# Kernel optimization log

Measured on AMD Instinct MI355X. Metric: run time of the kernel, lower is better.

## Reference

```python
import jax, jax.numpy as jnp
import numpy as np
import math

B, S, D, NH, HFF, E, K, C, L, V = 8, 256, 1024, 16, 2048, 8, 2, 10, 4, 32000
HD = D // NH
EPS = 1e-5


def _pos_encoding(max_len, d_model):
    pos = jnp.arange(max_len, dtype=jnp.float32)[:, None]
    div = jnp.exp(jnp.arange(0, d_model, 2, dtype=jnp.float32) * (-math.log(10000.0) / d_model))
    pe = jnp.zeros((max_len, d_model), dtype=jnp.float32)
    pe = pe.at[:, 0::2].set(jnp.sin(pos * div))
    pe = pe.at[:, 1::2].set(jnp.cos(pos * div))
    return pe[:, None, :]  # [max_len, 1, D], matching torch buffer layout


def _layernorm(x, g, b):
    mu = jnp.mean(x, axis=-1, keepdims=True)
    var = jnp.mean((x - mu) ** 2, axis=-1, keepdims=True)
    return (x - mu) * jax.lax.rsqrt(var + EPS) * g + b


def setup_inputs() -> dict:
    key = jax.random.key(0)
    ks = jax.random.split(key, 20)
    sc = lambda *shape: 0.02
    inp = {
        "src": jax.random.randint(ks[0], (B, S), 0, V, dtype=jnp.int32),
        "emb": jax.random.normal(ks[1], (V, D), jnp.float32) * 0.02,
        "in_proj_w": jax.random.normal(ks[2], (L, 3 * D, D), jnp.float32) * 0.02,
        "in_proj_b": jnp.zeros((L, 3 * D), jnp.float32),
        "out_w": jax.random.normal(ks[3], (L, D, D), jnp.float32) * 0.02,
        "out_b": jnp.zeros((L, D), jnp.float32),
        "ln1_g": jnp.ones((L, D), jnp.float32),
        "ln1_b": jnp.zeros((L, D), jnp.float32),
        "ln2_g": jnp.ones((L, D), jnp.float32),
        "ln2_b": jnp.zeros((L, D), jnp.float32),
        "gate_w": jax.random.normal(ks[4], (L, E, D), jnp.float32) * 0.02,
        "gate_b": jnp.zeros((L, E), jnp.float32),
        "w1": jax.random.normal(ks[5], (L, E, D, HFF), jnp.float32) * 0.02,
        "b1": jnp.zeros((L, E, HFF), jnp.float32),
        "w2": jax.random.normal(ks[6], (L, E, HFF, D), jnp.float32) * 0.02,
        "b2": jnp.zeros((L, E, D), jnp.float32),
        "cls_w": jax.random.normal(ks[7], (C, D), jnp.float32) * 0.02,
        "cls_b": jnp.zeros((C,), jnp.float32),
    }
    return inp


def _attention(x, ipw, ipb, ow, ob):
    # x: [B,S,D]
    qkv = x @ ipw.T + ipb  # [B,S,3D]
    q, k, v = jnp.split(qkv, 3, axis=-1)
    q = q.reshape(B, S, NH, HD)
    k = k.reshape(B, S, NH, HD)
    v = v.reshape(B, S, NH, HD)
    scores = jnp.einsum("bqhd,bkhd->bhqk", q, k) / math.sqrt(HD)
    attn = jax.nn.softmax(scores, axis=-1)
    o = jnp.einsum("bhqk,bkhd->bqhd", attn, v).reshape(B, S, D)
    return o @ ow.T + ob


def _moe(x, gw, gb, w1, b1, w2, b2):
    # x: [B,S,D]; gw: [E,D]; w1: [E,D,H]; w2: [E,H,D]
    t = x.reshape(B * S, D)
    logits = t @ gw.T + gb  # [T,E]
    topv, topi = jax.lax.top_k(logits, K)  # [T,K]
    weights = jax.nn.softmax(topv, axis=-1)  # [T,K]
    # dense expert compute (small E, compute-bound), combine via top-k gather
    h = jax.nn.relu(jnp.einsum("td,edh->teh", t, w1) + b1)  # [T,E,H]
    y = jnp.einsum("teh,ehd->ted", h, w2) + b2  # [T,E,D]
    sel = jnp.take_along_axis(y, topi[:, :, None], axis=1)  # [T,K,D]
    out = jnp.sum(sel * weights[:, :, None], axis=1)  # [T,D]
    return out.reshape(B, S, D), logits.reshape(B, S, E)


def reference(src, emb, in_proj_w, in_proj_b, out_w, out_b, ln1_g, ln1_b,
              ln2_g, ln2_b, gate_w, gate_b, w1, b1, w2, b2, cls_w, cls_b):
    x = emb[src] * math.sqrt(D)  # [B,S,D]
    pe = _pos_encoding(5000, D)  # [max_len,1,D]
    # faithful to original: pe indexed by batch dim (x.size(0)), broadcast over seq
    x = x + pe[:B]  # [B,1,D] -> broadcast [B,S,D]
    all_gates = []
    for l in range(in_proj_w.shape[0]):
        a = _attention(x, in_proj_w[l], in_proj_b[l], out_w[l], out_b[l])
        x = _layernorm(x + a, ln1_g[l], ln1_b[l])
        m, g = _moe(x, gate_w[l], gate_b[l], w1[l], b1[l], w2[l], b2[l])
        x = _layernorm(x + m, ln2_g[l], ln2_b[l])
        all_gates.append(g)
    pooled = jnp.mean(x, axis=1)  # [B,D]
    out = pooled @ cls_w.T + cls_b  # [B,C]
    return out, jnp.stack(all_gates)  # ([B,C], [L,B,S,E])
```

## Files before the change

### kernel.cpp

```cpp
#include <hip/hip_runtime.h>
#include <math.h>

#define TKN 2048
#define DIM 1024
#define NHEAD 16
#define HDIM 64
#define HFF 2048
#define NE 8
#define TOPK 2
#define NCLS 10
#define NLAYER 4
#define SEQ 256
#define BATCH 8

typedef __attribute__((ext_vector_type(8))) _Float16 f16x8;
typedef __attribute__((ext_vector_type(4))) float f32x4;
typedef __attribute__((ext_vector_type(8))) unsigned short u16x8;

__device__ __forceinline__ unsigned short f2h(float v) {
  _Float16 h = (_Float16)v;
  return __builtin_bit_cast(unsigned short, h);
}
__device__ __forceinline__ float h2f(unsigned short u) {
  return (float)__builtin_bit_cast(_Float16, u);
}
__device__ __forceinline__ void fsplit(float v, unsigned short& hi, unsigned short& lo) {
  _Float16 h = (_Float16)v;
  hi = __builtin_bit_cast(unsigned short, h);
  lo = f2h(v - (float)h);
}

__device__ __forceinline__ void gload_lds16(const void* g, void* l) {
  __builtin_amdgcn_global_load_lds((__attribute__((address_space(1))) void*)g,
                                   (__attribute__((address_space(3))) void*)l,
                                   16, 0, 0);
}

__global__ __launch_bounds__(256) void k_embed(const int* __restrict__ src,
                                               const float* __restrict__ emb,
                                               float* __restrict__ x,
                                               unsigned short* __restrict__ xhi,
                                               unsigned short* __restrict__ xlo) {
  const int t = blockIdx.x;
  const int tid = threadIdx.x;
  const int b = t / SEQ;
  const int tok = src[t];
  const float* erow = emb + (size_t)tok * DIM;
  const size_t base = (size_t)t * DIM;
  const float cexp = -9.210340371976184f / 1024.0f;
#pragma unroll
  for (int j = 0; j < 4; ++j) {
    int d = tid + 256 * j;
    int i2 = d & ~1;
    float ang = (float)b * expf((float)i2 * cexp);
    float pe = (d & 1) ? cosf(ang) : sinf(ang);
    float v = erow[d] * 32.0f + pe;
    x[base + d] = v;
    fsplit(v, xhi[base + d], xlo[base + d]);
  }
}

template <bool LO>
__global__ __launch_bounds__(256) void k_cvt_split(const float* __restrict__ in,
                                                   unsigned short* __restrict__ ohi,
                                                   unsigned short* __restrict__ olo) {
  int i = blockIdx.x * 256 + threadIdx.x;
  float4 v = ((const float4*)in)[i];
  ushort4 h, l;
  fsplit(v.x, h.x, l.x); fsplit(v.y, h.y, l.y);
  fsplit(v.z, h.z, l.z); fsplit(v.w, h.w, l.w);
  ((ushort4*)ohi)[i] = h;
  if (LO) ((ushort4*)olo)[i] = l;
}

template <bool LO>
__global__ __launch_bounds__(256) void k_cvt_t2(const float* __restrict__ in,
                                                unsigned short* __restrict__ ohi,
                                                unsigned short* __restrict__ olo,
                                                int R, int Cc) {
  __shared__ float ts[64][33];
  const int t = threadIdx.x;
  const int c0 = blockIdx.x * 32, r0 = blockIdx.y * 64;
  const float* ip = in + (size_t)blockIdx.z * R * Cc;
  const size_t obase = (size_t)blockIdx.z * R * Cc;
  const int cc = t & 31, rr0 = t >> 5;
#pragma unroll
  for (int j = 0; j < 8; ++j)
    ts[rr0 + 8 * j][cc] = ip[(size_t)(r0 + rr0 + 8 * j) * Cc + c0 + cc];
  __syncthreads();
  const int c = t >> 3, rch = (t & 7) * 8;
  u16x8 hv, lv;
#pragma unroll
  for (int i = 0; i < 8; ++i) {
    unsigned short hi, lo;
    fsplit(ts[rch + i][c], hi, lo);
    hv[i] = hi; lv[i] = lo;
  }
  size_t o = obase + (size_t)(c0 + c) * R + r0 + rch;
  *(u16x8*)(ohi + o) = hv;
  if (LO) *(u16x8*)(olo + o) = lv;
}

template <int MODE, bool RELU, int OUTK, bool SPLIT>
__global__ __launch_bounds__(256) void k_mfma_gemm(
    const unsigned short* __restrict__ Ahi, const unsigned short* __restrict__ Alo,
    const unsigned short* __restrict__ Bhi, const unsigned short* __restrict__ Blo,
    const float* __restrict__ bias, void* __restrict__ out0, void* __restrict__ out1,
    int M, int N, int K,
    const int* __restrict__ slot_token, const int* __restrict__ offg) {
  constexpr int NP = SPLIT ? 2 : 1;
  __shared__ unsigned short U[2][NP][128 * 64];
  const int tid = threadIdx.x;
  const int w = tid >> 6, lane = tid & 63;
  const int bm = blockIdx.y * 128, bn = blockIdx.x * 128;
  int r0 = 0, rows = M, e = 0;
  if (MODE != 0) {
    e = blockIdx.z;
    r0 = offg[e];
    rows = offg[e + 1] - r0;
    if (bm >= rows) return;
  }
  const size_t bwb = (size_t)e * K * N;
  const float* biasq = bias + (size_t)e * N;

  const int lrow8 = lane >> 3;
  const int s = (lane & 7) ^ lrow8;
  const int chunk = (s & 3) * 8;
  const unsigned short* sp0[4];
  const unsigned short* sp1[4];
#pragma unroll
  for (int i = 0; i < 4; ++i) {
    int rloc = w * 32 + i * 8 + lrow8;
    int growA;
    if (MODE == 0) {
      growA = bm + rloc;
    } else {
      int rr = bm + rloc;
      if (rr >= rows) rr = rows - 1;
      growA = (MODE == 1) ? slot_token[r0 + rr] : (r0 + rr);
    }
    size_t aoff = (size_t)growA * K + chunk;
    size_t boff = bwb + (size_t)(bn + rloc) * K + chunk;
    if constexpr (SPLIT) {
      sp0[i] = (s < 4 ? Ahi : Alo) + aoff;
      sp1[i] = (s < 4 ? Bhi : Blo) + boff;
    } else {
      sp0[i] = (s < 4) ? (Ahi + aoff) : (Bhi + boff);
      sp1[i] = nullptr;
    }
  }

  f32x4 acc[4][4] = {};
  const int wr = w >> 1, wc = w & 1;
  const int lr = lane & 15, lg = lane >> 4;
  const int sw = lr & 7;
  unsigned aoffs[4], boffs[4];
#pragma unroll
  for (int m = 0; m < 4; ++m)
    aoffs[m] = (unsigned)((wr * 64 + m * 16 + lr) * 64 + ((lg ^ sw) * 8));
#pragma unroll
  for (int n = 0; n < 4; ++n)
    boffs[n] = (unsigned)((wc * 64 + n * 16 + lr) * 64 + ((lg ^ sw) * 8));

#pragma unroll
  for (int i = 0; i < 4; ++i) {
    gload_lds16(sp0[i], &U[0][0][(w * 32 + i * 8) * 64]);
    sp0[i] += 32;
    if constexpr (SPLIT) {
      gload_lds16(sp1[i], &U[0][1][(w * 32 + i * 8) * 64]);
      sp1[i] += 32;
    }
  }

  const int NT = K / 32;
#pragma unroll 2
  for (int t = 0; t < NT; ++t) {
    const int cur = t & 1;
    if (t + 1 < NT) {
#pragma unroll
      for (int i = 0; i < 4; ++i) {
        gload_lds16(sp0[i], &U[cur ^ 1][0][(w * 32 + i * 8) * 64]);
        sp0[i] += 32;
        if constexpr (SPLIT) {
          gload_lds16(sp1[i], &U[cur ^ 1][1][(w * 32 + i * 8) * 64]);
          sp1[i] += 32;
        }
      }
      if constexpr (SPLIT)
        asm volatile("s_waitcnt vmcnt(8)" ::: "memory");
      else
        asm volatile("s_waitcnt vmcnt(4)" ::: "memory");
    } else {
      asm volatile("s_waitcnt vmcnt(0)" ::: "memory");
    }
    __builtin_amdgcn_s_barrier();

    f16x8 afh[4], bfh[4], afl[4], bfl[4];
    if constexpr (SPLIT) {
#pragma unroll
      for (int m = 0; m < 4; ++m) afh[m] = *(const f16x8*)&U[cur][0][aoffs[m]];
#pragma unroll
      for (int m = 0; m < 4; ++m) afl[m] = *(const f16x8*)&U[cur][0][aoffs[m] ^ 32];
#pragma unroll
      for (int n = 0; n < 4; ++n) bfh[n] = *(const f16x8*)&U[cur][1][boffs[n]];
#pragma unroll
      for (int n = 0; n < 4; ++n) bfl[n] = *(const f16x8*)&U[cur][1][boffs[n] ^ 32];
    } else {
#pragma unroll
      for (int m = 0; m < 4; ++m) afh[m] = *(const f16x8*)&U[cur][0][aoffs[m]];
#pragma unroll
      for (int n = 0; n < 4; ++n) bfh[n] = *(const f16x8*)&U[cur][0][boffs[n] ^ 32];
    }
#pragma unroll
    for (int m = 0; m < 4; ++m)
#pragma unroll
      for (int n = 0; n < 4; ++n) {
        acc[m][n] = __builtin_amdgcn_mfma_f32_16x16x32_f16(afh[m], bfh[n], acc[m][n], 0, 0, 0);
        if constexpr (SPLIT) {
          acc[m][n] = __builtin_amdgcn_mfma_f32_16x16x32_f16(afh[m], bfl[n], acc[m][n], 0, 0, 0);
          acc[m][n] = __builtin_amdgcn_mfma_f32_16x16x32_f16(afl[m], bfh[n], acc[m][n], 0, 0, 0);
        }
      }
    __builtin_amdgcn_s_barrier();
  }

  float bv[4];
#pragma unroll
  for (int n = 0; n < 4; ++n) bv[n] = biasq[bn + wc * 64 + n * 16 + lr];

#pragma unroll
  for (int m = 0; m < 4; ++m) {
#pragma unroll
    for (int j = 0; j < 4; ++j) {
      int rowg = bm + wr * 64 + m * 16 + lg * 4 + j;
      if (MODE != 0 && rowg >= rows) continue;
      size_t crow = (size_t)((MODE == 0) ? rowg : (r0 + rowg)) * N;
#pragma unroll
      for (int n = 0; n < 4; ++n) {
        float v = acc[m][n][j] + bv[n];
        if (RELU) v = fmaxf(v, 0.f);
        size_t o = crow + bn + wc * 64 + n * 16 + lr;
        if (OUTK == 0) {
          ((float*)out0)[o] = v;
        } else if (OUTK == 1) {
          ((unsigned short*)out0)[o] = f2h(v);
        } else {
          unsigned short hi, lo;
          fsplit(v, hi, lo);
          ((unsigned short*)out0)[o] = hi;
          ((unsigned short*)out1)[o] = lo;
        }
      }
    }
  }
}

__global__ __launch_bounds__(256) void k_attn(const float* __restrict__ qkv,
                                              unsigned short* __restrict__ ohi,
                                              unsigned short* __restrict__ olo) {
  const int qt = blockIdx.x;
  const int hh = blockIdx.y;
  const int bb = blockIdx.z;
  const int tid = threadIdx.x;
  __shared__ float qs[16][64];
  __shared__ float ps[16][256];
  const int t0 = bb * SEQ + qt * 16;
  for (int i = tid; i < 16 * 64; i += 256) {
    int qi = i >> 6, d = i & 63;
    qs[qi][d] = qkv[(size_t)(t0 + qi) * (3 * DIM) + hh * 64 + d];
  }
  __syncthreads();
  float s[16];
#pragma unroll
  for (int qi = 0; qi < 16; ++qi) s[qi] = 0.f;
  const float* krow = qkv + (size_t)(bb * SEQ + tid) * (3 * DIM) + DIM + hh * 64;
#pragma unroll 4
  for (int c = 0; c < 16; ++c) {
    float4 kv = *(const float4*)(krow + c * 4);
#pragma unroll
    for (int qi = 0; qi < 16; ++qi) {
      s[qi] += kv.x * qs[qi][c * 4 + 0] + kv.y * qs[qi][c * 4 + 1] +
               kv.z * qs[qi][c * 4 + 2] + kv.w * qs[qi][c * 4 + 3];
    }
  }
#pragma unroll
  for (int qi = 0; qi < 16; ++qi) ps[qi][tid] = s[qi] * 0.125f;
  __syncthreads();
  const int wv = tid >> 6, lane = tid & 63;
  for (int rr = wv; rr < 16; rr += 4) {
    float v[4];
#pragma unroll
    for (int j = 0; j < 4; ++j) v[j] = ps[rr][lane + 64 * j];
    float m = fmaxf(fmaxf(v[0], v[1]), fmaxf(v[2], v[3]));
    for (int msk = 32; msk; msk >>= 1) m = fmaxf(m, __shfl_xor(m, msk));
    float e[4], sum = 0.f;
#pragma unroll
    for (int j = 0; j < 4; ++j) { e[j] = expf(v[j] - m); sum += e[j]; }
    for (int msk = 32; msk; msk >>= 1) sum += __shfl_xor(sum, msk);
    float inv = 1.0f / sum;
#pragma unroll
    for (int j = 0; j < 4; ++j) ps[rr][lane + 64 * j] = e[j] * inv;
  }
  __syncthreads();
  const int qi0 = tid >> 6, d = tid & 63;
  float acc[4] = {0.f, 0.f, 0.f, 0.f};
  const float* vbase = qkv + (size_t)(bb * SEQ) * (3 * DIM) + 2 * DIM + hh * 64 + d;
  for (int k = 0; k < 256; ++k) {
    float vv = vbase[(size_t)k * (3 * DIM)];
    acc[0] += ps[qi0][k] * vv;
    acc[1] += ps[qi0 + 4][k] * vv;
    acc[2] += ps[qi0 + 8][k] * vv;
    acc[3] += ps[qi0 + 12][k] * vv;
  }
#pragma unroll
  for (int j = 0; j < 4; ++j) {
    size_t o = (size_t)(t0 + qi0 + 4 * j) * DIM + hh * 64 + d;
    fsplit(acc[j], ohi[o], olo[o]);
  }
}

__device__ __forceinline__ float block_reduce_sum(float v, float* red) {
  const int tid = threadIdx.x;
  red[tid] = v;
  __syncthreads();
  for (int s = 128; s > 0; s >>= 1) {
    if (tid < s) red[tid] += red[tid + s];
    __syncthreads();
  }
  float r = red[0];
  __syncthreads();
  return r;
}

__global__ __launch_bounds__(256) void k_add_ln_gate(const float* __restrict__ xin,
                                                     const float* __restrict__ add,
                                                     const float* __restrict__ g,
                                                     const float* __restrict__ bt,
                                                     const float* __restrict__ gw,
                                                     const float* __restrict__ gb,
                                                     float* __restrict__ xout,
                                                     unsigned short* __restrict__ xhi,
                                                     unsigned short* __restrict__ xlo,
                                                     float* __restrict__ gout,
                                                     int* __restrict__ topi,
                                                     float* __restrict__ topw) {
  __shared__ float red[256];
  __shared__ float pw[4][NE];
  __shared__ float lgs[NE];
  const int t = blockIdx.x, tid = threadIdx.x;
  const size_t base = (size_t)t * DIM;
  float v[4];
  float s = 0.f;
#pragma unroll
  for (int j = 0; j < 4; ++j) {
    int d = tid + 256 * j;
    v[j] = xin[base + d] + add[base + d];
    s += v[j];
  }
  float mean = block_reduce_sum(s, red) * (1.0f / DIM);
  float s2 = 0.f;
#pragma unroll
  for (int j = 0; j < 4; ++j) { float dv = v[j] - mean; s2 += dv * dv; }
  float var = block_reduce_sum(s2, red) * (1.0f / DIM);
  float rs = rsqrtf(var + 1e-5f);
  float o[4];
#pragma unroll
  for (int j = 0; j < 4; ++j) {
    int d = tid + 256 * j;
    o[j] = (v[j] - mean) * rs * g[d] + bt[d];
    xout[base + d] = o[j];
    fsplit(o[j], xhi[base + d], xlo[base + d]);
  }
  const int wv = tid >> 6, lane = tid & 63;
  float p[NE];
#pragma unroll
  for (int e = 0; e < NE; ++e) {
    float pe = 0.f;
#pragma unroll
    for (int j = 0; j < 4; ++j) pe += o[j] * gw[(size_t)e * DIM + tid + 256 * j];
    for (int m = 32; m; m >>= 1) pe += __shfl_xor(pe, m);
    p[e] = pe;
  }
  if (lane == 0) {
#pragma unroll
    for (int e = 0; e < NE; ++e) pw[wv][e] = p[e];
  }
  __syncthreads();
  if (tid < NE) {
    float l = pw[0][tid] + pw[1][tid] + pw[2][tid] + pw[3][tid] + gb[tid];
    gout[(size_t)t * NE + tid] = l;
    lgs[tid] = l;
  }
  __syncthreads();
  if (tid == 0) {
    int i0 = 0; float v0 = lgs[0];
    for (int i = 1; i < NE; ++i) if (lgs[i] > v0) { v0 = lgs[i]; i0 = i; }
    int i1 = -1; float v1 = -1e30f;
    for (int i = 0; i < NE; ++i) { if (i == i0) continue; if (lgs[i] > v1) { v1 = lgs[i]; i1 = i; } }
    float e1 = expf(v1 - v0);
    float w0 = 1.0f / (1.0f + e1);
    topi[2 * t] = i0; topi[2 * t + 1] = i1;
    topw[2 * t] = w0; topw[2 * t + 1] = e1 * w0;
  }
}

__global__ __launch_bounds__(512) void k_route(const int* __restrict__ topi,
                                               int* __restrict__ offg,
                                               int* __restrict__ slot_token,
                                               int* __restrict__ slot_of) {
  __shared__ int cnt_s[NE];
  __shared__ int off_s[NE + 1];
  const int tid = threadIdx.x;
  const int w = tid >> 6, lane = tid & 63;
  int c = 0;
  for (int i = lane; i < TKN * TOPK; i += 64) c += (topi[i] == w) ? 1 : 0;
  for (int m = 32; m; m >>= 1) c += __shfl_xor(c, m);
  if (lane == 0) cnt_s[w] = c;
  __syncthreads();
  if (tid == 0) {
    off_s[0] = 0;
    for (int e2 = 0; e2 < NE; ++e2) off_s[e2 + 1] = off_s[e2] + cnt_s[e2];
    for (int e2 = 0; e2 <= NE; ++e2) offg[e2] = off_s[e2];
  }
  __syncthreads();
  int base = off_s[w];
  for (int i0 = 0; i0 < TKN * TOPK; i0 += 64) {
    int i = i0 + lane;
    bool mm = (topi[i] == w);
    unsigned long long mask = __ballot(mm ? 1 : 0);
    int rank = __popcll(mask & ((1ull << lane) - 1ull));
    if (mm) {
      int slot = base + rank;
      slot_token[slot] = i >> 1;
      slot_of[i] = slot;
    }
    base += __popcll(mask);
  }
}

__global__ __launch_bounds__(256) void k_moe_combine_ln(const float* __restrict__ xin,
                                                        const float* __restrict__ y,
                                                        const float* __restrict__ topw,
                                                        const int* __restrict__ slot_of,
                                                        const float* __restrict__ g,
                                                        const float* __restrict__ bt,
                                                        float* __restrict__ xout,
                                                        unsigned short* __restrict__ xhi,
                                                        unsigned short* __restrict__ xlo) {
  __shared__ float red[256];
  const int t = blockIdx.x, tid = threadIdx.x;
  const float w0 = topw[2 * t], w1v = topw[2 * t + 1];
  const int s0 = slot_of[2 * t], s1 = slot_of[2 * t + 1];
  const size_t base = (size_t)t * DIM;
  float v[4];
  float s = 0.f;
#pragma unroll
  for (int j = 0; j < 4; ++j) {
    int d = tid + 256 * j;
    v[j] = xin[base + d] + w0 * y[(size_t)s0 * DIM + d] + w1v * y[(size_t)s1 * DIM + d];
    s += v[j];
  }
  float mean = block_reduce_sum(s, red) * (1.0f / DIM);
  float s2 = 0.f;
#pragma unroll
  for (int j = 0; j < 4; ++j) { float dv = v[j] - mean; s2 += dv * dv; }
  float var = block_reduce_sum(s2, red) * (1.0f / DIM);
  float rs = rsqrtf(var + 1e-5f);
#pragma unroll
  for (int j = 0; j < 4; ++j) {
    int d = tid + 256 * j;
    float o = (v[j] - mean) * rs * g[d] + bt[d];
    xout[base + d] = o;
    fsplit(o, xhi[base + d], xlo[base + d]);
  }
}

__global__ __launch_bounds__(256) void k_pool_cls(const float* __restrict__ x,
                                                  const float* __restrict__ cw,
                                                  const float* __restrict__ cb,
                                                  float* __restrict__ out) {
  __shared__ float pooled[DIM];
  const int b = blockIdx.x, tid = threadIdx.x;
  float a[4] = {0.f, 0.f, 0.f, 0.f};
  for (int s = 0; s < SEQ; ++s) {
    const float* row = x + (size_t)(b * SEQ + s) * DIM;
#pragma unroll
    for (int j = 0; j < 4; ++j) a[j] += row[tid + 256 * j];
  }
#pragma unroll
  for (int j = 0; j < 4; ++j) pooled[tid + 256 * j] = a[j] * (1.0f / SEQ);
  __syncthreads();
  const int wv = tid >> 6, lane = tid & 63;
  for (int c = wv; c < NCLS; c += 4) {
    float p = 0.f;
    for (int d = lane; d < DIM; d += 64) p += pooled[d] * cw[(size_t)c * DIM + d];
    for (int m = 32; m; m >>= 1) p += __shfl_xor(p, m);
    if (lane == 0) out[b * NCLS + c] = p + cb[c];
  }
}

extern "C" void kernel_launch(void* const* d_in, const int* in_sizes, int n_in,
                              void* d_out, int out_size, void* d_ws, size_t ws_size,
                              hipStream_t stream) {
  const int*   src  = (const int*)  d_in[0];
  const float* emb  = (const float*)d_in[1];
  const float* ipw  = (const float*)d_in[2];
  const float* ipb  = (const float*)d_in[3];
  const float* ow   = (const float*)d_in[4];
  const float* ob   = (const float*)d_in[5];
  const float* ln1g = (const float*)d_in[6];
  const float* ln1b = (const float*)d_in[7];
  const float* ln2g = (const float*)d_in[8];
  const float* ln2b = (const float*)d_in[9];
  const float* gw   = (const float*)d_in[10];
  const float* gb   = (const float*)d_in[11];
  const float* w1   = (const float*)d_in[12];
  const float* b1   = (const float*)d_in[13];
  const float* w2   = (const float*)d_in[14];
  const float* b2   = (const float*)d_in[15];
  const float* cw   = (const float*)d_in[16];
  const float* cb   = (const float*)d_in[17];
  float* out = (float*)d_out;

  char* ws = (char*)d_ws;
  size_t off = 0;
  auto carve = [&](size_t bytes) -> void* {
    void* p = ws + off;
    off += (bytes + 255) & ~(size_t)255;
    return p;
  };
  float*          x     = (float*)carve((size_t)TKN * DIM * 4);
  unsigned short* xhi   = (unsigned short*)carve((size_t)TKN * DIM * 2);
  unsigned short* xlo   = (unsigned short*)carve((size_t)TKN * DIM * 2);
  char*           bufQ  = (char*)carve((size_t)2 * TKN * TOPK * HFF * 2);
  float*          qkv   = (float*)bufQ;
  unsigned short* h_hi  = (unsigned short*)bufQ;
  unsigned short* h_lo  = (unsigned short*)(bufQ + (size_t)TKN * TOPK * HFF * 2);
  unsigned short* at_hi = (unsigned short*)carve((size_t)TKN * DIM * 2);
  unsigned short* at_lo = (unsigned short*)carve((size_t)TKN * DIM * 2);
  char*           bufP  = (char*)carve((size_t)TKN * TOPK * DIM * 4);
  float*          proj  = (float*)bufP;
  float*          ybuf  = (float*)bufP;
  unsigned short* wq_hi = (unsigned short*)carve((size_t)3 * DIM * DIM * 2);
  unsigned short* wq_lo = (unsigned short*)carve((size_t)3 * DIM * DIM * 2);
  unsigned short* wo_hi = (unsigned short*)carve((size_t)DIM * DIM * 2);
  unsigned short* wo_lo = (unsigned short*)carve((size_t)DIM * DIM * 2);
  unsigned short* wt_hi = (unsigned short*)carve((size_t)NE * DIM * HFF * 2);
  unsigned short* wt_lo = (unsigned short*)carve((size_t)NE * DIM * HFF * 2);
  float* topw       = (float*)carve((size_t)TKN * TOPK * 4);
  int*   topi       = (int*)  carve((size_t)TKN * TOPK * 4);
  int*   slot_token = (int*)  carve((size_t)TKN * TOPK * 4);
  int*   slot_of    = (int*)  carve((size_t)TKN * TOPK * 4);
  int*   offg       = (int*)  carve(64);

  k_embed<<<TKN, 256, 0, stream>>>(src, emb, x, xhi, xlo);

  for (int l = 0; l < NLAYER; ++l) {
    const float* ipw_l = ipw + (size_t)l * 3 * DIM * DIM;
    const float* ow_l  = ow  + (size_t)l * DIM * DIM;
    const float* w1_l  = w1  + (size_t)l * NE * DIM * HFF;
    const float* w2_l  = w2  + (size_t)l * NE * HFF * DIM;
    const bool spd = (l < 3);
    const bool spm = (l < 2);

    if (spd) {
      k_cvt_split<true><<<(3 * DIM * DIM) / 1024, 256, 0, stream>>>(ipw_l, wq_hi, wq_lo);
      k_cvt_split<true><<<(DIM * DIM) / 1024, 256, 0, stream>>>(ow_l, wo_hi, wo_lo);
    } else {
      k_cvt_split<false><<<(3 * DIM * DIM) / 1024, 256, 0, stream>>>(ipw_l, wq_hi, wq_lo);
      k_cvt_split<false><<<(DIM * DIM) / 1024, 256, 0, stream>>>(ow_l, wo_hi, wo_lo);
    }
    if (spm)
      k_cvt_t2<true><<<dim3(HFF / 32, DIM / 64, NE), 256, 0, stream>>>(w1_l, wt_hi, wt_lo, DIM, HFF);
    else
      k_cvt_t2<false><<<dim3(HFF / 32, DIM / 64, NE), 256, 0, stream>>>(w1_l, wt_hi, wt_lo, DIM, HFF);

    if (spd)
      k_mfma_gemm<0, false, 0, true><<<dim3(3 * DIM / 128, TKN / 128), 256, 0, stream>>>(
          xhi, xlo, wq_hi, wq_lo, ipb + (size_t)l * 3 * DIM, qkv, nullptr, TKN, 3 * DIM, DIM, nullptr, nullptr);
    else
      k_mfma_gemm<0, false, 0, false><<<dim3(3 * DIM / 128, TKN / 128), 256, 0, stream>>>(
          xhi, xlo, wq_hi, wq_lo, ipb + (size_t)l * 3 * DIM, qkv, nullptr, TKN, 3 * DIM, DIM, nullptr, nullptr);

    k_attn<<<dim3(SEQ / 16, NHEAD, BATCH), 256, 0, stream>>>(qkv, at_hi, at_lo);

    if (spd)
      k_mfma_gemm<0, false, 0, true><<<dim3(DIM / 128, TKN / 128), 256, 0, stream>>>(
          at_hi, at_lo, wo_hi, wo_lo, ob + (size_t)l * DIM, proj, nullptr, TKN, DIM, DIM, nullptr, nullptr);
    else
      k_mfma_gemm<0, false, 0, false><<<dim3(DIM / 128, TKN / 128), 256, 0, stream>>>(
          at_hi, at_lo, wo_hi, wo_lo, ob + (size_t)l * DIM, proj, nullptr, TKN, DIM, DIM, nullptr, nullptr);

    k_add_ln_gate<<<TKN, 256, 0, stream>>>(x, proj, ln1g + l * DIM, ln1b + l * DIM,
                                           gw + (size_t)l * NE * DIM, gb + l * NE,
                                           x, xhi, xlo,
                                           out + NCLS * BATCH + (size_t)l * TKN * NE, topi, topw);
    k_route<<<1, 512, 0, stream>>>(topi, offg, slot_token, slot_of);

    if (spm)
      k_mfma_gemm<1, true, 2, true><<<dim3(HFF / 128, TKN * TOPK / 128, NE), 256, 0, stream>>>(
          xhi, xlo, wt_hi, wt_lo, b1 + (size_t)l * NE * HFF, h_hi, h_lo, 0, HFF, DIM, slot_token, offg);
    else
      k_mfma_gemm<1, true, 1, false><<<dim3(HFF / 128, TKN * TOPK / 128, NE), 256, 0, stream>>>(
          xhi, xlo, wt_hi, wt_lo, b1 + (size_t)l * NE * HFF, h_hi, nullptr, 0, HFF, DIM, slot_token, offg);

    if (spm)
      k_cvt_t2<true><<<dim3(DIM / 32, HFF / 64, NE), 256, 0, stream>>>(w2_l, wt_hi, wt_lo, HFF, DIM);
    else
      k_cvt_t2<false><<<dim3(DIM / 32, HFF / 64, NE), 256, 0, stream>>>(w2_l, wt_hi, wt_lo, HFF, DIM);

    if (spm)
      k_mfma_gemm<2, false, 0, true><<<dim3(DIM / 128, TKN * TOPK / 128, NE), 256, 0, stream>>>(
          h_hi, h_lo, wt_hi, wt_lo, b2 + (size_t)l * NE * DIM, ybuf, nullptr, 0, DIM, HFF, nullptr, offg);
    else
      k_mfma_gemm<2, false, 0, false><<<dim3(DIM / 128, TKN * TOPK / 128, NE), 256, 0, stream>>>(
          h_hi, h_lo, wt_hi, wt_lo, b2 + (size_t)l * NE * DIM, ybuf, nullptr, 0, DIM, HFF, nullptr, offg);

    k_moe_combine_ln<<<TKN, 256, 0, stream>>>(x, ybuf, topw, slot_of,
                                              ln2g + l * DIM, ln2b + l * DIM, x, xhi, xlo);
  }
  k_pool_cls<<<BATCH, 256, 0, stream>>>(x, cw, cb, out);
}
```

Before: 1.455 ms.

## Use 32x32 MFMA in GEMM and MFMA-based QK^T with split-fp16 in attention

The GEMM inner tile switches from 16x16x32 MFMA with a 4x4 accumulator grid to 32x32x16 MFMA with a 2x2 grid. LDS fragment offsets and the epilogue row mapping are adjusted to match. The attention kernel now computes QK^T with split hi/lo fp16 MFMA, reading Q and K directly from global memory, instead of scalar FMA over an LDS copy of Q. The PV loop also reads probabilities as float4 vectors. The aim is to cut LDS traffic and instruction count, at the cost of new layout-mapping risks and somewhat different rounding in the score computation.

```diff
diff --git a/kernel.cpp b/kernel.cpp
--- a/kernel.cpp
+++ b/kernel.cpp
@@ -15,19 +15,26 @@
 
 typedef __attribute__((ext_vector_type(8))) _Float16 f16x8;
 typedef __attribute__((ext_vector_type(4))) float f32x4;
+typedef __attribute__((ext_vector_type(16))) float f32x16;
 typedef __attribute__((ext_vector_type(8))) unsigned short u16x8;
 
 __device__ __forceinline__ unsigned short f2h(float v) {
   _Float16 h = (_Float16)v;
   return __builtin_bit_cast(unsigned short, h);
-}
-__device__ __forceinline__ float h2f(unsigned short u) {
-  return (float)__builtin_bit_cast(_Float16, u);
 }
 __device__ __forceinline__ void fsplit(float v, unsigned short& hi, unsigned short& lo) {
   _Float16 h = (_Float16)v;
   hi = __builtin_bit_cast(unsigned short, h);
   lo = f2h(v - (float)h);
+}
+__device__ __forceinline__ void split8(float4 f0, float4 f1, f16x8& h, f16x8& l) {
+  float fv[8] = {f0.x, f0.y, f0.z, f0.w, f1.x, f1.y, f1.z, f1.w};
+#pragma unroll
+  for (int i = 0; i < 8; ++i) {
+    _Float16 hh = (_Float16)fv[i];
+    h[i] = hh;
+    l[i] = (_Float16)(fv[i] - (float)hh);
+  }
 }
 
 __device__ __forceinline__ void gload_lds16(const void* g, void* l) {
@@ -150,17 +157,21 @@
     }
   }
 
-  f32x4 acc[4][4] = {};
+  f32x16 acc[2][2] = {};
   const int wr = w >> 1, wc = w & 1;
-  const int lr = lane & 15, lg = lane >> 4;
-  const int sw = lr & 7;
-  unsigned aoffs[4], boffs[4];
-#pragma unroll
-  for (int m = 0; m < 4; ++m)
-    aoffs[m] = (unsigned)((wr * 64 + m * 16 + lr) * 64 + ((lg ^ sw) * 8));
-#pragma unroll
-  for (int n = 0; n < 4; ++n)
-    boffs[n] = (unsigned)((wc * 64 + n * 16 + lr) * 64 + ((lg ^ sw) * 8));
+  const int l31 = lane & 31, kq = lane >> 5;
+  const int sw = lane & 7;
+  unsigned aof[2][2], bof[2][2];
+#pragma unroll
+  for (int mt = 0; mt < 2; ++mt)
+#pragma unroll
+    for (int kh = 0; kh < 2; ++kh)
+      aof[mt][kh] = (unsigned)((wr * 64 + mt * 32 + l31) * 64 + (((kh * 2 + kq) ^ sw) * 8));
+#pragma unroll
+  for (int nt = 0; nt < 2; ++nt)
+#pragma unroll
+    for (int kh = 0; kh < 2; ++kh)
+      bof[nt][kh] = (unsigned)((wc * 64 + nt * 32 + l31) * 64 + (((kh * 2 + kq) ^ sw) * 8));
 
 #pragma unroll
   for (int i = 0; i < 4; ++i) {
@@ -195,51 +206,57 @@
     }
     __builtin_amdgcn_s_barrier();
 
-    f16x8 afh[4], bfh[4], afl[4], bfl[4];
-    if constexpr (SPLIT) {
-#pragma unroll
-      for (int m = 0; m < 4; ++m) afh[m] = *(const f16x8*)&U[cur][0][aoffs[m]];
-#pragma unroll
-      for (int m = 0; m < 4; ++m) afl[m] = *(const f16x8*)&U[cur][0][aoffs[m] ^ 32];
-#pragma unroll
-      for (int n = 0; n < 4; ++n) bfh[n] = *(const f16x8*)&U[cur][1][boffs[n]];
-#pragma unroll
-      for (int n = 0; n < 4; ++n) bfl[n] = *(const f16x8*)&U[cur][1][boffs[n] ^ 32];
-    } else {
-#pragma unroll
-      for (int m = 0; m < 4; ++m) afh[m] = *(const f16x8*)&U[cur][0][aoffs[m]];
-#pragma unroll
-      for (int n = 0; n < 4; ++n) bfh[n] = *(const f16x8*)&U[cur][0][boffs[n] ^ 32];
-    }
-#pragma unroll
-    for (int m = 0; m < 4; ++m)
-#pragma unroll
-      for (int n = 0; n < 4; ++n) {
-        acc[m][n] = __builtin_amdgcn_mfma_f32_16x16x32_f16(afh[m], bfh[n], acc[m][n], 0, 0, 0);
+    f16x8 Ah[2][2], Bh[2][2], Al[2][2], Bl[2][2];
+#pragma unroll
+    for (int mt = 0; mt < 2; ++mt)
+#pragma unroll
+      for (int kh = 0; kh < 2; ++kh) {
+        Ah[mt][kh] = *(const f16x8*)&U[cur][0][aof[mt][kh]];
+        if constexpr (SPLIT) Al[mt][kh] = *(const f16x8*)&U[cur][0][aof[mt][kh] ^ 32];
+      }
+#pragma unroll
+    for (int nt = 0; nt < 2; ++nt)
+#pragma unroll
+      for (int kh = 0; kh < 2; ++kh) {
         if constexpr (SPLIT) {
-          acc[m][n] = __builtin_amdgcn_mfma_f32_16x16x32_f16(afh[m], bfl[n], acc[m][n], 0, 0, 0);
-          acc[m][n] = __builtin_amdgcn_mfma_f32_16x16x32_f16(afl[m], bfh[n], acc[m][n], 0, 0, 0);
+          Bh[nt][kh] = *(const f16x8*)&U[cur][1][bof[nt][kh]];
+          Bl[nt][kh] = *(const f16x8*)&U[cur][1][bof[nt][kh] ^ 32];
+        } else {
+          Bh[nt][kh] = *(const f16x8*)&U[cur][0][bof[nt][kh] ^ 32];
         }
       }
+#pragma unroll
+    for (int mt = 0; mt < 2; ++mt)
+#pragma unroll
+      for (int nt = 0; nt < 2; ++nt)
+#pragma unroll
+        for (int kh = 0; kh < 2; ++kh) {
+          acc[mt][nt] = __builtin_amdgcn_mfma_f32_32x32x16_f16(Ah[mt][kh], Bh[nt][kh], acc[mt][nt], 0, 0, 0);
+          if constexpr (SPLIT) {
+            acc[mt][nt] = __builtin_amdgcn_mfma_f32_32x32x16_f16(Ah[mt][kh], Bl[nt][kh], acc[mt][nt], 0, 0, 0);
+            acc[mt][nt] = __builtin_amdgcn_mfma_f32_32x32x16_f16(Al[mt][kh], Bh[nt][kh], acc[mt][nt], 0, 0, 0);
+          }
+        }
     __builtin_amdgcn_s_barrier();
   }
 
-  float bv[4];
-#pragma unroll
-  for (int n = 0; n < 4; ++n) bv[n] = biasq[bn + wc * 64 + n * 16 + lr];
-
-#pragma unroll
-  for (int m = 0; m < 4; ++m) {
-#pragma unroll
-    for (int j = 0; j < 4; ++j) {
-      int rowg = bm + wr * 64 + m * 16 + lg * 4 + j;
+  float bv[2];
+#pragma unroll
+  for (int nt = 0; nt < 2; ++nt) bv[nt] = biasq[bn + wc * 64 + nt * 32 + l31];
+
+#pragma unroll
+  for (int mt = 0; mt < 2; ++mt) {
+#pragma unroll
+    for (int reg = 0; reg < 16; ++reg) {
+      int rloc = (reg & 3) + 8 * (reg >> 2) + 4 * kq;
+      int rowg = bm + wr * 64 + mt * 32 + rloc;
       if (MODE != 0 && rowg >= rows) continue;
       size_t crow = (size_t)((MODE == 0) ? rowg : (r0 + rowg)) * N;
 #pragma unroll
-      for (int n = 0; n < 4; ++n) {
-        float v = acc[m][n][j] + bv[n];
+      for (int nt = 0; nt < 2; ++nt) {
+        float v = acc[mt][nt][reg] + bv[nt];
         if (RELU) v = fmaxf(v, 0.f);
-        size_t o = crow + bn + wc * 64 + n * 16 + lr;
+        size_t o = crow + bn + wc * 64 + nt * 32 + l31;
         if (OUTK == 0) {
           ((float*)out0)[o] = v;
         } else if (OUTK == 1) {
@@ -258,36 +275,41 @@
 __global__ __launch_bounds__(256) void k_attn(const float* __restrict__ qkv,
                                               unsigned short* __restrict__ ohi,
                                               unsigned short* __restrict__ olo) {
-  const int qt = blockIdx.x;
-  const int hh = blockIdx.y;
-  const int bb = blockIdx.z;
-  const int tid = threadIdx.x;
-  __shared__ float qs[16][64];
   __shared__ float ps[16][256];
+  const int qt = blockIdx.x, hh = blockIdx.y, bb = blockIdx.z;
+  const int tid = threadIdx.x, w = tid >> 6, lane = tid & 63;
+  const int lr = lane & 15, lg = lane >> 4;
   const int t0 = bb * SEQ + qt * 16;
-  for (int i = tid; i < 16 * 64; i += 256) {
-    int qi = i >> 6, d = i & 63;
-    qs[qi][d] = qkv[(size_t)(t0 + qi) * (3 * DIM) + hh * 64 + d];
-  }
-  __syncthreads();
-  float s[16];
-#pragma unroll
-  for (int qi = 0; qi < 16; ++qi) s[qi] = 0.f;
-  const float* krow = qkv + (size_t)(bb * SEQ + tid) * (3 * DIM) + DIM + hh * 64;
-#pragma unroll 4
-  for (int c = 0; c < 16; ++c) {
-    float4 kv = *(const float4*)(krow + c * 4);
-#pragma unroll
-    for (int qi = 0; qi < 16; ++qi) {
-      s[qi] += kv.x * qs[qi][c * 4 + 0] + kv.y * qs[qi][c * 4 + 1] +
-               kv.z * qs[qi][c * 4 + 2] + kv.w * qs[qi][c * 4 + 3];
-    }
-  }
-#pragma unroll
-  for (int qi = 0; qi < 16; ++qi) ps[qi][tid] = s[qi] * 0.125f;
-  __syncthreads();
-  const int wv = tid >> 6, lane = tid & 63;
-  for (int rr = wv; rr < 16; rr += 4) {
+
+  f16x8 qh[2], ql[2];
+#pragma unroll
+  for (int kh = 0; kh < 2; ++kh) {
+    const float* qb = qkv + (size_t)(t0 + lr) * (3 * DIM) + hh * 64 + kh * 32 + lg * 8;
+    split8(*(const float4*)qb, *(const float4*)(qb + 4), qh[kh], ql[kh]);
+  }
+#pragma unroll
+  for (int nt = 0; nt < 4; ++nt) {
+    f16x8 kvh[2], kvl[2];
+#pragma unroll
+    for (int kh = 0; kh < 2; ++kh) {
+      const float* kb = qkv + (size_t)(bb * SEQ + w * 64 + nt * 16 + lr) * (3 * DIM)
+                        + DIM + hh * 64 + kh * 32 + lg * 8;
+      split8(*(const float4*)kb, *(const float4*)(kb + 4), kvh[kh], kvl[kh]);
+    }
+    f32x4 a = {0.f, 0.f, 0.f, 0.f};
+#pragma unroll
+    for (int kh = 0; kh < 2; ++kh) {
+      a = __builtin_amdgcn_mfma_f32_16x16x32_f16(qh[kh], kvh[kh], a, 0, 0, 0);
+      a = __builtin_amdgcn_mfma_f32_16x16x32_f16(qh[kh], kvl[kh], a, 0, 0, 0);
+      a = __builtin_amdgcn_mfma_f32_16x16x32_f16(ql[kh], kvh[kh], a, 0, 0, 0);
+    }
+#pragma unroll
+    for (int j = 0; j < 4; ++j)
+      ps[lg * 4 + j][w * 64 + nt * 16 + lr] = a[j] * 0.125f;
+  }
+  __syncthreads();
+
+  for (int rr = w; rr < 16; rr += 4) {
     float v[4];
 #pragma unroll
     for (int j = 0; j < 4; ++j) v[j] = ps[rr][lane + 64 * j];
@@ -302,20 +324,30 @@
     for (int j = 0; j < 4; ++j) ps[rr][lane + 64 * j] = e[j] * inv;
   }
   __syncthreads();
-  const int qi0 = tid >> 6, d = tid & 63;
-  float acc[4] = {0.f, 0.f, 0.f, 0.f};
+
+  const int qi0 = w, d = lane;
+  float a0 = 0.f, a1 = 0.f, a2 = 0.f, a3 = 0.f;
   const float* vbase = qkv + (size_t)(bb * SEQ) * (3 * DIM) + 2 * DIM + hh * 64 + d;
-  for (int k = 0; k < 256; ++k) {
-    float vv = vbase[(size_t)k * (3 * DIM)];
-    acc[0] += ps[qi0][k] * vv;
-    acc[1] += ps[qi0 + 4][k] * vv;
-    acc[2] += ps[qi0 + 8][k] * vv;
-    acc[3] += ps[qi0 + 12][k] * vv;
-  }
+  for (int k4 = 0; k4 < 64; ++k4) {
+    float4 p0 = *(const float4*)&ps[qi0][k4 * 4];
+    float4 p1 = *(const float4*)&ps[qi0 + 4][k4 * 4];
+    float4 p2 = *(const float4*)&ps[qi0 + 8][k4 * 4];
+    float4 p3 = *(const float4*)&ps[qi0 + 12][k4 * 4];
+    float q0[4] = {p0.x, p0.y, p0.z, p0.w};
+    float q1[4] = {p1.x, p1.y, p1.z, p1.w};
+    float q2[4] = {p2.x, p2.y, p2.z, p2.w};
+    float q3[4] = {p3.x, p3.y, p3.z, p3.w};
+#pragma unroll
+    for (int j = 0; j < 4; ++j) {
+      float vv = vbase[(size_t)(k4 * 4 + j) * (3 * DIM)];
+      a0 += q0[j] * vv; a1 += q1[j] * vv; a2 += q2[j] * vv; a3 += q3[j] * vv;
+    }
+  }
+  float accs[4] = {a0, a1, a2, a3};
 #pragma unroll
   for (int j = 0; j < 4; ++j) {
     size_t o = (size_t)(t0 + qi0 + 4 * j) * DIM + hh * 64 + d;
-    fsplit(acc[j], ohi[o], olo[o]);
+    fsplit(accs[j], ohi[o], olo[o]);
   }
 }
 
```

Result: no change. 1.447 ms (-0.5%).
